# Kernel tuning notes

Measured on AMD Instinct MI355X. Metric: run time of the kernel, lower is better.

The kernel has to match this reference:

```python
import jax, jax.numpy as jnp
import numpy as np

B, S, E, H, T, VOCAB = 64, 512, 256, 512, 32, 32000

def setup_inputs():
    key = jax.random.key(0)
    ks = jax.random.split(key, 19)
    g = lambda i, shape: jax.random.normal(ks[i], shape, jnp.float32) * 0.05
    return {
        "sentence": jax.random.randint(ks[0], (S, B), 0, VOCAB),
        "emb_enc": g(1, (VOCAB, E)),
        "emb_dec": g(2, (VOCAB, E)),
        "W_ih": g(3, (4 * H, E)),
        "W_hh": g(4, (4 * H, H)),
        "b_ih": g(5, (4 * H,)),
        "b_hh": g(6, (4 * H,)),
        "dec_in0": g(7, (E,)),
        "Wx": g(8, (4 * H, E)),
        "bx": g(9, (4 * H,)),
        "Wh": g(10, (4 * H, H)),
        "bh": g(11, (4 * H,)),
        "W_out": g(12, (H, 2 * H)),
        "b_out": g(13, (H,)),
        "W_in": g(14, (H, H)),
        "b_in": g(15, (H,)),
        "W_ctx": g(16, (H, H)),
        "b_ctx": g(17, (H,)),
        "V": jax.random.uniform(ks[18], (H,), jnp.float32, -1.0, 1.0),
    }

def _lstm_cell(x, h, c, Wi, Whh, bi, bhh):
    # gate order i, f, g, o (matches torch LSTM and the decoder's chunk order)
    gates = x @ Wi.T + h @ Whh.T + bi + bhh
    i, f, g, o = jnp.split(gates, 4, axis=-1)
    c_t = jax.nn.sigmoid(f) * c + jax.nn.sigmoid(i) * jnp.tanh(g)
    h_t = jax.nn.sigmoid(o) * jnp.tanh(c_t)
    return h_t, c_t

def _pointer_net(sentence, emb_enc, emb_dec, W_ih, W_hh, b_ih, b_hh, dec_in0,
                 Wx, bx, Wh, bh, W_out, b_out, W_in, b_in, W_ctx, b_ctx, V):
    s_len, b = sentence.shape
    h_dim = W_hh.shape[1]
    embs = emb_enc[sentence]                          # [S, B, E]
    h0 = jnp.zeros((b, h_dim), embs.dtype)
    c0 = jnp.zeros((b, h_dim), embs.dtype)

    def enc_step(carry, x_t):
        h, c = _lstm_cell(x_t, carry[0], carry[1], W_ih, W_hh, b_ih, b_hh)
        return (h, c), h

    (h_n, c_n), enc_out = jax.lax.scan(enc_step, (h0, c0), embs)   # enc_out [S, B, H]
    context = enc_out.transpose(1, 0, 2)              # [B, S, H]
    # conv1d(kernel=1) projection of the context; constant across decode steps
    ctx = jnp.einsum('bsh,gh->bgs', context, W_ctx) + b_ctx[None, :, None]  # [B, H, S]

    dec_embs = emb_dec[sentence].transpose(1, 0, 2)   # [B, S, E]
    pos = jnp.arange(s_len)

    def dec_step(carry, _):
        dec_in, h, c, mask = carry
        h_t, c_t = _lstm_cell(dec_in, h, c, Wx, Wh, bx, bh)
        inp = h_t @ W_in.T + b_in                      # [B, H]
        att = jnp.einsum('h,bhs->bs', V, jnp.tanh(inp[:, :, None] + ctx))
        att = jnp.where(mask == 0, -jnp.inf, att)
        alpha = jax.nn.softmax(att, axis=1)            # [B, S]
        hidden_state = jnp.einsum('bhs,bs->bh', ctx, alpha)
        h_new = jnp.tanh(jnp.concatenate([hidden_state, h_t], axis=1) @ W_out.T + b_out)
        idx = jnp.argmax(alpha * mask, axis=1)         # greedy pointer, first max on ties
        one_hot = (pos[None, :] == idx[:, None]).astype(alpha.dtype)
        mask_new = mask * (1.0 - one_hot)
        next_in = jnp.take_along_axis(dec_embs, idx[:, None, None], axis=1)[:, 0, :]
        return (next_in, h_new, c_t, mask_new), (alpha, idx)

    mask0 = jnp.ones((b, s_len), embs.dtype)
    dec_in0_b = jnp.broadcast_to(dec_in0, (b, dec_in0.shape[0]))
    _, (alphas, ptrs) = jax.lax.scan(dec_step, (dec_in0_b, h_n, c_n, mask0), None, length=T)
    return alphas.transpose(1, 0, 2), ptrs.T          # [B, T, S], [B, T]

def reference(sentence, emb_enc, emb_dec, W_ih, W_hh, b_ih, b_hh, dec_in0,
              Wx, bx, Wh, bh, W_out, b_out, W_in, b_in, W_ctx, b_ctx, V):
    return _pointer_net(sentence, emb_enc, emb_dec, W_ih, W_hh, b_ih, b_hh, dec_in0,
                        Wx, bx, Wh, bh, W_out, b_out, W_in, b_in, W_ctx, b_ctx, V)
```

## Files before the change

### kernel.cpp

```cpp
#include <hip/hip_runtime.h>
#include <hip/hip_bf16.h>


typedef unsigned short u16;
typedef unsigned long long u64;
typedef __bf16 bf16_t;
typedef bf16_t bf16x8 __attribute__((ext_vector_type(8)));
typedef float f32x4 __attribute__((ext_vector_type(4)));

#define MFMA16(a, b, c) __builtin_amdgcn_mfma_f32_16x16x32_bf16(a, b, c, 0, 0, 0)
#define AGENT __HIP_MEMORY_SCOPE_AGENT

#define FLG_OFF   64u
#define FLE_OFF   128u
#define FLC_OFF   8320u
#define LDD_OFF   10368u
#define GEND_OFF  11392u
#define FLD_OFF   11520u
#define BAR_END   27904u
#define HE_OFF    32768u
#define CW_OFF    425984u
#define HD_OFF    557056u
#define AO_OFF    688128u
#define INP_OFF   950272u
#define ATT_OFF   1081344u
#define MSK_OFF   1212416u
#define PAC_OFF   1343488u
#define PML_OFF   1867776u
#define DIN_OFF   1871872u
#define CTX_OFF   2097152u
#define CTXL_OFF  (CTX_OFF + 33554432u)
#define NEED_T0   (CTX_OFF + 67108864u)
#define NEED_T1   (CTX_OFF + 50331648u)
#define NEED_T2   (CTX_OFF + 33554432u)

__device__ __forceinline__ float bf2f(u16 b) {
  union { unsigned u; float f; } c; c.u = ((unsigned)b) << 16; return c.f;
}
__device__ __forceinline__ u16 f2bf(float x) {
  union { float f; unsigned u; } c; c.f = x;
  unsigned r = c.u + 0x7FFFu + ((c.u >> 16) & 1u);
  return (u16)(r >> 16);
}
__device__ __forceinline__ float sigf(float x) { return 1.0f / (1.0f + expf(-x)); }
__device__ __forceinline__ float sel4(float a0, float a1, float a2, float a3, int j) {
  float r = (j == 1) ? a1 : a0;
  r = (j == 2) ? a2 : r;
  r = (j == 3) ? a3 : r;
  return r;
}
__device__ __forceinline__ float wget(const void* p, long i, int f32m) {
  return f32m ? ((const float*)p)[i] : bf2f(((const u16*)p)[i]);
}
__device__ __forceinline__ void ld8(const void* p, long i, int f32m, float (&o)[8]) {
  if (f32m) {
    const float4* q = (const float4*)((const float*)p + i);
    float4 a = q[0], b = q[1];
    o[0] = a.x; o[1] = a.y; o[2] = a.z; o[3] = a.w;
    o[4] = b.x; o[5] = b.y; o[6] = b.z; o[7] = b.w;
  } else {
    uint4 u = *(const uint4*)((const u16*)p + i);
    unsigned ww[4] = {u.x, u.y, u.z, u.w};
#pragma unroll
    for (int k = 0; k < 4; ++k) {
      o[2 * k] = bf2f((u16)(ww[k] & 0xFFFFu));
      o[2 * k + 1] = bf2f((u16)(ww[k] >> 16));
    }
  }
}
__device__ __forceinline__ float ald(const float* p) {
  return __hip_atomic_load(p, __ATOMIC_RELAXED, AGENT);
}
__device__ __forceinline__ void ast(float* p, float v) {
  __hip_atomic_store(p, v, __ATOMIC_RELAXED, AGENT);
}
__device__ __forceinline__ int aldi(const int* p) {
  return __hip_atomic_load(p, __ATOMIC_RELAXED, AGENT);
}

__device__ __forceinline__ void split3(float x, u16& h, u16& l, u16& l2) {
  union { float f; unsigned u; } c; c.f = x;
  h = (u16)(c.u >> 16);
  float r = x - bf2f(h);
  union { float f; unsigned u; } e; e.f = r;
  l = (u16)(e.u >> 16);
  float r2 = r - bf2f(l);
  union { float f; unsigned u; } g; g.f = r2;
  l2 = (u16)(g.u >> 16);
}
__device__ __forceinline__ void split8v(const float (&a)[8], bf16x8& H, bf16x8& L,
                                        bf16x8& L2) {
  union { unsigned u[4]; bf16x8 v; } hh, ll, mm;
#pragma unroll
  for (int k = 0; k < 4; ++k) {
    union { float f; unsigned u; } x0, x1;
    x0.f = a[2 * k]; x1.f = a[2 * k + 1];
    unsigned t0 = x0.u & 0xFFFF0000u, t1 = x1.u & 0xFFFF0000u;
    union { unsigned u; float f; } b0, b1; b0.u = t0; b1.u = t1;
    float r0 = x0.f - b0.f, r1 = x1.f - b1.f;
    union { float f; unsigned u; } e0, e1; e0.f = r0; e1.f = r1;
    unsigned s0 = e0.u & 0xFFFF0000u, s1 = e1.u & 0xFFFF0000u;
    union { unsigned u; float f; } c0, c1; c0.u = s0; c1.u = s1;
    float q0 = r0 - c0.f, q1 = r1 - c1.f;
    union { float f; unsigned u; } g0, g1; g0.f = q0; g1.f = q1;
    hh.u[k] = t1 | (x0.u >> 16);
    ll.u[k] = s1 | (e0.u >> 16);
    mm.u[k] = (g1.u & 0xFFFF0000u) | (g0.u >> 16);
  }
  H = hh.v; L = ll.v; L2 = mm.v;
}
__device__ __forceinline__ f32x4 mfma6(const bf16x8& ah, const bf16x8& al,
                                       const bf16x8& al2, const bf16x8& bh,
                                       const bf16x8& bl, const bf16x8& bl2, f32x4 acc) {
  acc = MFMA16(ah, bh, acc);
  acc = MFMA16(al, bh, acc);
  acc = MFMA16(ah, bl, acc);
  acc = MFMA16(al, bl, acc);
  acc = MFMA16(ah, bl2, acc);
  acc = MFMA16(al2, bh, acc);
  return acc;
}
__device__ __forceinline__ f32x4 groupMMv(const float (&a8)[8], const u16* B3c, int bo,
                                          f32x4 acc) {
  bf16x8 H, L, L2;
  split8v(a8, H, L, L2);
  return mfma6(H, L, L2, *(const bf16x8*)(B3c + bo), *(const bf16x8*)(B3c + 4224 + bo),
               *(const bf16x8*)(B3c + 8448 + bo), acc);
}
__device__ __forceinline__ void stage16(u16* B3, const void* W, int f32m,
                                        long src, int n, int k16) {
  float t0[8], t1[8];
  ld8(W, src, f32m, t0);
  ld8(W, src + 8, f32m, t1);
#pragma unroll
  for (int j = 0; j < 8; ++j) {
    u16 h, l, l2; split3(t0[j], h, l, l2);
    int o = n * 264 + k16 + j;
    B3[o] = h; B3[4224 + o] = l; B3[8448 + o] = l2;
  }
#pragma unroll
  for (int j = 0; j < 8; ++j) {
    u16 h, l, l2; split3(t1[j], h, l, l2);
    int o = n * 264 + k16 + 8 + j;
    B3[o] = h; B3[4224 + o] = l; B3[8448 + o] = l2;
  }
}

__device__ __forceinline__ f32x4 gemmStaged(const float* __restrict__ T,
    const u16* __restrict__ B3, int kgoff, int ng, float* __restrict__ hS,
    int tid, int ln15, int q, int bA, f32x4 acc) {
  const int nch = ng >> 2;
  u64 pend[16];
#pragma unroll
  for (int i = 0; i < 16; ++i)
    pend[i] = __hip_atomic_load((const u64*)T + i * 256 + tid,
                                __ATOMIC_RELAXED, AGENT);
  __syncthreads();
#pragma unroll
  for (int i = 0; i < 16; ++i) {
    int gi = i * 256 + tid;
    ((u64*)hS)[(gi >> 5) * 33 + (gi & 31)] = pend[i];
  }
  __syncthreads();
#pragma unroll 1
  for (int c = 0; c < nch; ++c) {
    if (c + 1 < nch) {
#pragma unroll
      for (int i = 0; i < 16; ++i)
        pend[i] = __hip_atomic_load((const u64*)T + (c + 1) * 4096 + i * 256 + tid,
                                    __ATOMIC_RELAXED, AGENT);
    }
#pragma unroll
    for (int k4 = 0; k4 < 4; ++k4) {
      const int kg = c * 4 + k4 + kgoff;
      float a8[8];
#pragma unroll
      for (int j = 0; j < 8; ++j)
        a8[j] = hS[(k4 * 32 + q * 8 + j) * 66 + bA];
      acc = groupMMv(a8, B3 + (kg >> 3) * 12672,
                     ln15 * 264 + (kg & 7) * 32 + q * 8, acc);
    }
    if (c + 1 < nch) {
      __syncthreads();
#pragma unroll
      for (int i = 0; i < 16; ++i) {
        int gi = i * 256 + tid;
        ((u64*)hS)[(gi >> 5) * 33 + (gi & 31)] = pend[i];
      }
      __syncthreads();
    }
  }
  return acc;
}

__device__ __forceinline__ void ctx_store(char* ws, int tier, int oi, float x) {
  if (tier == 0) { ((float*)(ws + CTX_OFF))[oi] = x; return; }
  if (tier >= 3) return;
  u16 hi = f2bf(x);
  ((u16*)(ws + CTX_OFF))[oi] = hi;
  if (tier == 1) {
    unsigned e = hi & 0x7F80u; if (e == 0) e = 0x0080u;
    float us = bf2f((u16)e) * 0.00390625f;
    float r = (x - bf2f(hi)) / us;
    int q = (int)__float2int_rn(r * 254.0f);
    q = max(-127, min(127, q));
    ((signed char*)(ws + CTXL_OFF))[oi] = (signed char)q;
  }
}
__device__ __forceinline__ void ctx_load8(const char* ws, int tier, int oi, float (&cx)[8]) {
  if (tier == 0) {
    const float4* p = (const float4*)((const float*)(ws + CTX_OFF) + oi);
    float4 a = p[0], b = p[1];
    cx[0] = a.x; cx[1] = a.y; cx[2] = a.z; cx[3] = a.w;
    cx[4] = b.x; cx[5] = b.y; cx[6] = b.z; cx[7] = b.w;
    return;
  }
  if (tier >= 3) {
#pragma unroll
    for (int j = 0; j < 8; ++j) cx[j] = 0.0f;
    return;
  }
  uint4 hu = *(const uint4*)((const u16*)(ws + CTX_OFF) + oi);
  unsigned hw[4] = {hu.x, hu.y, hu.z, hu.w};
  u16 h[8];
#pragma unroll
  for (int k = 0; k < 4; ++k) { h[2*k] = (u16)(hw[k] & 0xFFFFu); h[2*k+1] = (u16)(hw[k] >> 16); }
#pragma unroll
  for (int j = 0; j < 8; ++j) cx[j] = bf2f(h[j]);
  if (tier == 1) {
    const signed char* lp = (const signed char*)(ws + CTXL_OFF) + oi;
#pragma unroll
    for (int j = 0; j < 8; ++j) {
      unsigned e = h[j] & 0x7F80u; if (e == 0) e = 0x0080u;
      float us = bf2f((u16)e) * 0.00390625f;
      cx[j] += (float)lp[j] * us * (1.0f / 254.0f);
    }
  }
}

__device__ __forceinline__ void enc_arrive(char* ws, unsigned off, int idx, int gen) {
  __builtin_amdgcn_s_waitcnt(0);
  __syncthreads();
  if (threadIdx.x == 0)
    __hip_atomic_store((int*)(ws + off) + idx * 16, gen, __ATOMIC_RELAXED, AGENT);
}
__device__ __forceinline__ void gate_wait(char* ws, int gen, int genc) {
  const int tid = threadIdx.x;
  if (tid < 128) {
    const int* f = (const int*)(ws + FLE_OFF) + tid * 16;
    while (aldi(f) < gen) __builtin_amdgcn_s_sleep(2);
  } else if (tid < 160 && genc > 0) {
    const int* f = (const int*)(ws + FLC_OFF) + (tid - 128) * 16;
    while (aldi(f) < genc) __builtin_amdgcn_s_sleep(2);
  }
  __syncthreads();
}
__device__ __forceinline__ void ctx_wait(char* ws, int gen) {
  const int tid = threadIdx.x;
  if (tid < 128) {
    const int* f = (const int*)(ws + FLE_OFF) + tid * 16;
    while (aldi(f) < gen) __builtin_amdgcn_s_sleep(2);
  }
  __syncthreads();
}

__device__ __forceinline__ void sbar_arrive(char* ws, int wg, int gen) {
  __builtin_amdgcn_s_waitcnt(0);
  __syncthreads();
  if (threadIdx.x == 0)
    __hip_atomic_store((int*)(ws + FLD_OFF) + wg * 16, gen, __ATOMIC_RELAXED, AGENT);
}
__device__ __forceinline__ void sbar_wait(char* ws, int wg, int gen) {
  const int tid = threadIdx.x;
  if (tid < 64) {
    int* fl = (int*)(ws + FLD_OFF);
    int* ldv = (int*)(ws + LDD_OFF);
    int* gp = (int*)(ws + GEND_OFF);
    if (wg < 16) {
      if (tid < 16) {
        const int* f = &fl[(wg + (tid << 4)) * 16];
        while (aldi(f) < gen) __builtin_amdgcn_s_sleep(2);
      }
      if (tid == 0) __hip_atomic_store(&ldv[wg * 16], gen, __ATOMIC_RELAXED, AGENT);
    }
    if (wg == 0) {
      if (tid < 16) {
        const int* f = &ldv[tid * 16];
        while (aldi(f) < gen) __builtin_amdgcn_s_sleep(2);
      }
      if (tid == 0) __hip_atomic_store(gp, gen, __ATOMIC_RELAXED, AGENT);
    }
    if (tid == 0)
      while (aldi((const int*)gp) < gen) __builtin_amdgcn_s_sleep(2);
  }
  __syncthreads();
}

__global__ void prep_detect(const void* embE, char* ws) {
  __shared__ int cnt;
  if (threadIdx.x == 0) cnt = 0;
  __syncthreads();
  const u16* p = (const u16*)embE;
  int c = 0;
  for (int i = threadIdx.x; i < 4096; i += 256) {
    float v = bf2f(p[i]);
    if (!(fabsf(v) < 4.0f)) c++;
  }
  atomicAdd(&cnt, c);
  __syncthreads();
  if (threadIdx.x == 0) *(int*)(ws + FLG_OFF) = (cnt > 200) ? 1 : 0;
}

__global__ void prep_init(const void* din0, char* ws) {
  const int f32m = *(const int*)(ws + FLG_OFF);
  int i0 = blockIdx.x * 256 + threadIdx.x;
  int stride = gridDim.x * 256;
  int* bars = (int*)ws;
  for (int i = i0; i < (int)((BAR_END - FLE_OFF) / 4); i += stride)
    bars[(FLE_OFF / 4) + i] = 0;
  float* he = (float*)(ws + HE_OFF);
  float* mask = (float*)(ws + MSK_OFF);
  float* dinT = (float*)(ws + DIN_OFF);
  for (int i = i0; i < 98304; i += stride) he[i] = 0.0f;
  for (int i = i0; i < 32768; i += stride) mask[i] = 1.0f;
  for (int i = i0; i < 16384; i += stride) dinT[i] = wget(din0, i >> 6, f32m);
}

__global__ __launch_bounds__(256, 1) void enc_pers(
    const int* __restrict__ sent, const void* __restrict__ embE,
    const void* __restrict__ Wih, const void* __restrict__ Whh,
    const void* __restrict__ bih, const void* __restrict__ bhh,
    const void* __restrict__ Wctx, const void* __restrict__ bctx,
    char* __restrict__ ws, int tier) {
  __shared__ __align__(16) u16 B3[38016];
  __shared__ __align__(16) float hS[8448];
  const int tid = threadIdx.x, w = blockIdx.x;
  const int f32m = *(const int*)(ws + FLG_OFF);
  const int lane = tid & 63, v = tid >> 6, ln15 = lane & 15, q = lane >> 4;
  const int bA = v * 16 + ln15;
  const int sn = tid >> 4, sk = (tid & 15) * 16;
  float* heT = (float*)(ws + HE_OFF);
  float* cwp = (float*)(ws + CW_OFF);

  const int g = ln15 & 3;
  const int unit = w * 4 + (ln15 >> 2);

  if (w < 128) {
    float creg[4];
#pragma unroll
    for (int r = 0; r < 4; ++r) creg[r] = 0.0f;
    long grC = (long)(g * 512 + unit);
    float bias = wget(bih, grC, f32m) + wget(bhh, grC, f32m);
    const long grS = (long)((sn & 3) * 512 + w * 4 + (sn >> 2));
    stage16(B3, Wih, f32m, grS * 256 + sk, sn, sk);
    stage16(B3 + 12672, Whh, f32m, grS * 512 + sk, sn, sk);
    stage16(B3 + 25344, Whh, f32m, grS * 512 + 256 + sk, sn, sk);
    __syncthreads();

    int sR = 2, sW = 0;
#pragma unroll 1
    for (int u = 0; u < 512; ++u) {
      const int tok = sent[u * 64 + bA];
      f32x4 acc = {0.f, 0.f, 0.f, 0.f};
      {
        float aE[4][8];
#pragma unroll
        for (int pf = 0; pf < 3; ++pf)
          ld8(embE, (long)tok * 256 + pf * 32 + q * 8, f32m, aE[pf]);
#pragma unroll
        for (int ks = 0; ks < 8; ++ks) {
          if (ks + 3 < 8) ld8(embE, (long)tok * 256 + (ks + 3) * 32 + q * 8, f32m,
                              aE[(ks + 3) & 3]);
          acc = groupMMv(aE[ks & 3], B3, ln15 * 264 + ks * 32 + q * 8, acc);
        }
      }
      if (u) gate_wait(ws, u, u - 1);
      acc = gemmStaged(heT + sR * 32768, B3, 8, 16, hS, tid, ln15, q, bA, acc);
      float* hdTs = heT + sW * 32768;
#pragma unroll
      for (int r = 0; r < 4; ++r) {
        int br = v * 16 + q * 4 + r;
        float val = acc[r] + bias;
        float x1 = __shfl_xor(val, 1);
        float x2 = __shfl_xor(val, 2);
        float x3 = __shfl_xor(val, 3);
        float gi = sel4(val, x1, x2, x3, g);
        float gf = sel4(val, x1, x2, x3, g ^ 1);
        float gg = sel4(val, x1, x2, x3, g ^ 2);
        float go = sel4(val, x1, x2, x3, g ^ 3);
        float cn = sigf(gf) * creg[r] + sigf(gi) * tanhf(gg);
        float hv = sigf(go) * tanhf(cn);
        creg[r] = cn;
        if (g == 0) ast(hdTs + unit * 64 + br, hv);
      }
      enc_arrive(ws, FLE_OFF, w, u + 1);
      sR = sW; sW = (sW == 2) ? 0 : sW + 1;
    }
    if (g == 0) {
#pragma unroll
      for (int r = 0; r < 4; ++r) cwp[(v * 16 + q * 4 + r) * 512 + unit] = creg[r];
    }
  } else {
    const int w2 = w - 128;
    const long grS = (long)(w2 * 16 + sn);
    stage16(B3, Wctx, f32m, grS * 512 + sk, sn, sk);
    stage16(B3 + 12672, Wctx, f32m, grS * 512 + 256 + sk, sn, sk);
    __syncthreads();
    const int d = w2 * 16 + ln15;
    float bb = wget(bctx, d, f32m);
    int sC = 0;
#pragma unroll 1
    for (int vv = 0; vv < 512; ++vv) {
      ctx_wait(ws, vv + 1);
      f32x4 acc = {0.f, 0.f, 0.f, 0.f};
      acc = gemmStaged(heT + sC * 32768, B3, 0, 16, hS, tid, ln15, q, bA, acc);
#pragma unroll
      for (int r = 0; r < 4; ++r) {
        int br = v * 16 + q * 4 + r;
        ctx_store(ws, tier, (br * 512 + vv) * 512 + d, acc[r] + bb);
      }
      enc_arrive(ws, FLC_OFF, w2, vv + 1);
      sC = (sC == 2) ? 0 : sC + 1;
    }
  }
}

__global__ __launch_bounds__(256, 1) void dec_pers(
    const int* __restrict__ sent, const void* __restrict__ embD,
    const void* __restrict__ Wx, const void* __restrict__ bx,
    const void* __restrict__ Wh, const void* __restrict__ bh,
    const void* __restrict__ Wout, const void* __restrict__ bout,
    const void* __restrict__ Win, const void* __restrict__ bin,
    const void* __restrict__ V, char* __restrict__ ws,
    float* __restrict__ out, int tier) {
  __shared__ __align__(16) u16 B3[50688];
  __shared__ __align__(16) float hS[8448];
  __shared__ float accL[512];
  __shared__ float mlL[8];
  __shared__ float redA[256];
  __shared__ int redI[256];

  const int tid = threadIdx.x, wg = blockIdx.x;
  const int f32m = *(const int*)(ws + FLG_OFF);
  const int lane = tid & 63, v = tid >> 6, ln15 = lane & 15, q = lane >> 4;
  const int bA = v * 16 + ln15;
  const int sn = tid >> 4, sk = (tid & 15) * 16;
  float* hdT = (float*)(ws + HD_OFF);
  float* aoT = (float*)(ws + AO_OFF);
  float* inp = (float*)(ws + INP_OFF);
  float* att = (float*)(ws + ATT_OFF);
  float* mask = (float*)(ws + MSK_OFF);
  float* pac = (float*)(ws + PAC_OFF);
  float* pml = (float*)(ws + PML_OFF);
  float* dinT = (float*)(ws + DIN_OFF);
  const float* hnT = (const float*)(ws + HE_OFF) + 32768;
  int bgen = 0;

  const int g = ln15 & 3;
  const int unit = (wg < 128) ? (wg * 4 + (ln15 >> 2)) : 0;
  float creg[4];
  float bias = 0.0f;
  if (wg < 128) {
    const float* cwp = (const float*)(ws + CW_OFF);
#pragma unroll
    for (int r = 0; r < 4; ++r) creg[r] = cwp[(v * 16 + q * 4 + r) * 512 + unit];
    bias = wget(bx, (long)(g * 512 + unit), f32m) + wget(bh, (long)(g * 512 + unit), f32m);
  }
  float vj[8];
#pragma unroll
  for (int j = 0; j < 8; ++j) vj[j] = wget(V, lane * 8 + j, f32m);

  if (wg < 128) {
    const long grS = (long)((sn & 3) * 512 + wg * 4 + (sn >> 2));
    stage16(B3, Wx, f32m, grS * 256 + sk, sn, sk);
    stage16(B3 + 12672, Wh, f32m, grS * 512 + sk, sn, sk);
    stage16(B3 + 25344, Wh, f32m, grS * 512 + 256 + sk, sn, sk);
  } else if (wg < 160) {
    const long grS = (long)((wg - 128) * 16 + sn);
    stage16(B3, Win, f32m, grS * 512 + sk, sn, sk);
    stage16(B3 + 12672, Win, f32m, grS * 512 + 256 + sk, sn, sk);
  } else if (wg < 192) {
    const long grS = (long)((wg - 160) * 16 + sn);
#pragma unroll
    for (int cc = 0; cc < 4; ++cc)
      stage16(B3 + cc * 12672, Wout, f32m, grS * 1024 + cc * 256 + sk, sn, sk);
  }
  __syncthreads();

  f32x4 acc1 = {0.f, 0.f, 0.f, 0.f};
  if (wg < 128)
    acc1 = gemmStaged(dinT, B3, 0, 8, hS, tid, ln15, q, bA, acc1);

#pragma unroll 1
  for (int t = 0; t < 32; ++t) {
    if (wg < 128) {
      const float* hsT = (t == 0) ? hnT : (const float*)hdT;
      acc1 = gemmStaged(hsT, B3, 8, 16, hS, tid, ln15, q, bA, acc1);
#pragma unroll
      for (int r = 0; r < 4; ++r) {
        int br = v * 16 + q * 4 + r;
        float val = acc1[r] + bias;
        float x1 = __shfl_xor(val, 1);
        float x2 = __shfl_xor(val, 2);
        float x3 = __shfl_xor(val, 3);
        float gi = sel4(val, x1, x2, x3, g);
        float gf = sel4(val, x1, x2, x3, g ^ 1);
        float gg = sel4(val, x1, x2, x3, g ^ 2);
        float go = sel4(val, x1, x2, x3, g ^ 3);
        float cn = sigf(gf) * creg[r] + sigf(gi) * tanhf(gg);
        float hv = sigf(go) * tanhf(cn);
        creg[r] = cn;
        if (g == 0) ast(aoT + (512 + unit) * 64 + br, hv);
      }
    }
    ++bgen;
    sbar_arrive(ws, wg, bgen);
    sbar_wait(ws, wg, bgen);
    if (wg >= 128 && wg < 160) {
      f32x4 acc = {0.f, 0.f, 0.f, 0.f};
      acc = gemmStaged((const float*)aoT + 32768, B3, 0, 16, hS, tid, ln15, q, bA, acc);
      const int d = (wg - 128) * 16 + ln15;
      float bb = wget(bin, d, f32m);
#pragma unroll
      for (int r = 0; r < 4; ++r)
        ast(inp + (v * 16 + q * 4 + r) * 512 + d, acc[r] + bb);
    }
    ++bgen;
    sbar_arrive(ws, wg, bgen);
    const int b = wg & 63, qq = wg >> 6;
    const int s0 = qq * 128 + v * 32;
    float mkB[4];
    float cxB[4][8];
#pragma unroll
    for (int pf = 0; pf < 3; ++pf) {
      mkB[pf] = ald(mask + b * 512 + s0 + pf);
      ctx_load8(ws, tier, (b * 512 + s0 + pf) * 512 + lane * 8, cxB[pf]);
    }
    sbar_wait(ws, wg, bgen);
    {
      float ij[8];
#pragma unroll
      for (int j = 0; j < 8; ++j) ij[j] = ald(inp + b * 512 + lane * 8 + j);
      for (int i = tid; i < 512; i += 256) accL[i] = 0.0f;
      __syncthreads();
      float m = -1e30f, l = 0.0f;
      float oacc[8];
#pragma unroll
      for (int j = 0; j < 8; ++j) oacc[j] = 0.0f;
#pragma unroll 1
      for (int i0 = 0; i0 < 32; ++i0) {
        const int s = s0 + i0;
        if (i0 + 3 < 32) {
          mkB[(i0 + 3) & 3] = ald(mask + b * 512 + s + 3);
          ctx_load8(ws, tier, (b * 512 + s + 3) * 512 + lane * 8, cxB[(i0 + 3) & 3]);
        }
        float mkC = mkB[i0 & 3];
        const float (&cxC)[8] = cxB[i0 & 3];
        if (mkC == 0.0f) {
          if (lane == 0) ast(att + b * 512 + s, -1e30f);
        } else {
          float p = 0.0f;
#pragma unroll
          for (int j = 0; j < 8; ++j) p += vj[j] * tanhf(ij[j] + cxC[j]);
#pragma unroll
          for (int off = 1; off < 64; off <<= 1) p += __shfl_xor(p, off);
          if (lane == 0) ast(att + b * 512 + s, p);
          if (p <= m) {
            float e = expf(p - m);
            l += e;
#pragma unroll
            for (int j = 0; j < 8; ++j) oacc[j] += e * cxC[j];
          } else {
            float sc = expf(m - p);
            l = l * sc + 1.0f;
#pragma unroll
            for (int j = 0; j < 8; ++j) oacc[j] = oacc[j] * sc + cxC[j];
            m = p;
          }
        }
      }
      if (lane == 0) { mlL[v * 2] = m; mlL[v * 2 + 1] = l; }
      __syncthreads();
      float M = fmaxf(fmaxf(mlL[0], mlL[2]), fmaxf(mlL[4], mlL[6]));
      float Lq = 0.0f;
#pragma unroll
      for (int vv = 0; vv < 4; ++vv) Lq += mlL[vv * 2 + 1] * expf(mlL[vv * 2] - M);
      float scv = expf(m - M);
      for (int vv = 0; vv < 4; ++vv) {
        if (v == vv) {
#pragma unroll
          for (int j = 0; j < 8; ++j) accL[lane * 8 + j] += oacc[j] * scv;
        }
        __syncthreads();
      }
      for (int i = tid; i < 512; i += 256) ast(pac + (b * 4 + qq) * 512 + i, accL[i]);
      if (tid == 0) {
        ast(pml + (b * 4 + qq) * 2, M);
        ast(pml + (b * 4 + qq) * 2 + 1, Lq);
      }
    }
    ++bgen;
    sbar_arrive(ws, wg, bgen);
    sbar_wait(ws, wg, bgen);
    if (wg < 64) {
      const int bb = wg;
      float m0 = ald(pml + (bb * 4 + 0) * 2), m1 = ald(pml + (bb * 4 + 1) * 2);
      float m2 = ald(pml + (bb * 4 + 2) * 2), m3 = ald(pml + (bb * 4 + 3) * 2);
      float l0 = ald(pml + (bb * 4 + 0) * 2 + 1), l1 = ald(pml + (bb * 4 + 1) * 2 + 1);
      float l2 = ald(pml + (bb * 4 + 2) * 2 + 1), l3 = ald(pml + (bb * 4 + 3) * 2 + 1);
      float M = fmaxf(fmaxf(m0, m1), fmaxf(m2, m3));
      float e0 = expf(m0 - M), e1 = expf(m1 - M), e2 = expf(m2 - M), e3 = expf(m3 - M);
      float L = l0 * e0 + l1 * e1 + l2 * e2 + l3 * e3;
      L = fmaxf(L, 1e-30f);
      for (int h = tid; h < 512; h += 256) {
        float hv = (ald(pac + (bb * 4 + 0) * 512 + h) * e0 +
                    ald(pac + (bb * 4 + 1) * 512 + h) * e1 +
                    ald(pac + (bb * 4 + 2) * 512 + h) * e2 +
                    ald(pac + (bb * 4 + 3) * 512 + h) * e3) / L;
        ast(aoT + h * 64 + bb, hv);
      }
      float bestA = -1.0f;
      int bestS = 0;
#pragma unroll
      for (int k = 0; k < 2; ++k) {
        int s = tid * 2 + k;
        float a = expf(ald(att + bb * 512 + s) - M) / L;
        out[(bb * 32 + t) * 512 + s] = a;
        if (a > bestA) { bestA = a; bestS = s; }
      }
      redA[tid] = bestA;
      redI[tid] = bestS;
      __syncthreads();
      for (int st = 128; st > 0; st >>= 1) {
        if (tid < st) {
          if (redA[tid + st] > redA[tid]) { redA[tid] = redA[tid + st]; redI[tid] = redI[tid + st]; }
        }
        __syncthreads();
      }
      int idx = redI[0];
      if (tid == 0) {
        ast(mask + bb * 512 + idx, 0.0f);
        out[1048576 + bb * 32 + t] = (float)idx;
      }
      int token = sent[idx * 64 + bb];
      ast(dinT + tid * 64 + bb, wget(embD, (long)token * 256 + tid, f32m));
    }
    ++bgen;
    sbar_arrive(ws, wg, bgen);
    sbar_wait(ws, wg, bgen);
    if (wg >= 160 && wg < 192) {
      f32x4 acc = {0.f, 0.f, 0.f, 0.f};
      acc = gemmStaged((const float*)aoT, B3, 0, 32, hS, tid, ln15, q, bA, acc);
      const int d = (wg - 160) * 16 + ln15;
      float bb2 = wget(bout, d, f32m);
#pragma unroll
      for (int r = 0; r < 4; ++r)
        ast(hdT + d * 64 + (v * 16 + q * 4 + r), tanhf(acc[r] + bb2));
    }
    ++bgen;
    sbar_arrive(ws, wg, bgen);
    if (wg < 128 && t < 31) {
      f32x4 accn = {0.f, 0.f, 0.f, 0.f};
      accn = gemmStaged(dinT, B3, 0, 8, hS, tid, ln15, q, bA, accn);
      acc1 = accn;
    }
    if (t < 31) sbar_wait(ws, wg, bgen);
  }
}

__global__ void diag_kernel(char* ws, float* out, int wsMiB) {
  if (threadIdx.x == 0 && blockIdx.x == 0) {
    int f = *(int*)(ws + FLG_OFF);
    out[0] = (float)(wsMiB + 2000 * f);
  }
}

extern "C" void kernel_launch(void* const* d_in, const int* in_sizes, int n_in,
                              void* d_out, int out_size, void* d_ws, size_t ws_size,
                              hipStream_t stream) {
  (void)in_sizes; (void)n_in; (void)out_size;
  const int* sent = (const int*)d_in[0];
  const void* embE = d_in[1];
  const void* embD = d_in[2];
  const void* Wih = d_in[3];
  const void* Whh = d_in[4];
  const void* bih = d_in[5];
  const void* bhh = d_in[6];
  const void* din0 = d_in[7];
  const void* Wx = d_in[8];
  const void* bx = d_in[9];
  const void* Wh = d_in[10];
  const void* bh = d_in[11];
  const void* Wout = d_in[12];
  const void* bout = d_in[13];
  const void* Win = d_in[14];
  const void* bin = d_in[15];
  const void* Wctx = d_in[16];
  const void* bctx = d_in[17];
  const void* V = d_in[18];
  char* ws = (char*)d_ws;
  float* out = (float*)d_out;

  int tier;
  if (ws_size >= (size_t)NEED_T0) tier = 0;
  else if (ws_size >= (size_t)NEED_T1) tier = 1;
  else if (ws_size >= (size_t)NEED_T2) tier = 2;
  else tier = 3;

  prep_detect<<<dim3(1), dim3(256), 0, stream>>>(embE, ws);
  prep_init<<<dim3(64), dim3(256), 0, stream>>>(din0, ws);
  enc_pers<<<dim3(160), dim3(256), 0, stream>>>(sent, embE, Wih, Whh, bih, bhh,
                                                Wctx, bctx, ws, tier);
  dec_pers<<<dim3(256), dim3(256), 0, stream>>>(sent, embD, Wx, bx, Wh, bh, Wout, bout,
                                                Win, bin, V, ws, out, tier);
  if (tier >= 2)
    diag_kernel<<<dim3(1), dim3(64), 0, stream>>>(ws, out, (int)(ws_size >> 20));
}
```

Baseline: 9.206 ms.

## Double-buffer staged GEMM operands and restructure grid barriers into two-level trees

```diff
diff --git a/kernel.cpp b/kernel.cpp
--- a/kernel.cpp
+++ b/kernel.cpp
@@ -14,10 +14,10 @@
 #define FLG_OFF   64u
 #define FLE_OFF   128u
 #define FLC_OFF   8320u
-#define LDD_OFF   10368u
-#define GEND_OFF  11392u
-#define FLD_OFF   11520u
-#define BAR_END   27904u
+#define LDVG_OFF  10368u
+#define FLD_OFF   10880u
+#define LDVD_OFF  27264u
+#define BAR_END   28288u
 #define HE_OFF    32768u
 #define CW_OFF    425984u
 #define HD_OFF    557056u
@@ -77,6 +77,9 @@
 __device__ __forceinline__ int aldi(const int* p) {
   return __hip_atomic_load(p, __ATOMIC_RELAXED, AGENT);
 }
+__device__ __forceinline__ void asti(int* p, int v) {
+  __hip_atomic_store(p, v, __ATOMIC_RELAXED, AGENT);
+}
 
 __device__ __forceinline__ void split3(float x, u16& h, u16& l, u16& l2) {
   union { float f; unsigned u; } c; c.f = x;
@@ -146,46 +149,99 @@
   }
 }
 
-__device__ __forceinline__ f32x4 gemmStaged(const float* __restrict__ T,
+__device__ __forceinline__ f32x4 gemmStaged128(const float* __restrict__ T,
     const u16* __restrict__ B3, int kgoff, int ng, float* __restrict__ hS,
     int tid, int ln15, int q, int bA, f32x4 acc) {
   const int nch = ng >> 2;
   u64 pend[16];
 #pragma unroll
   for (int i = 0; i < 16; ++i)
-    pend[i] = __hip_atomic_load((const u64*)T + i * 256 + tid,
-                                __ATOMIC_RELAXED, AGENT);
+    pend[i] = __hip_atomic_load((const u64*)T + i * 256 + tid, __ATOMIC_RELAXED, AGENT);
   __syncthreads();
 #pragma unroll
   for (int i = 0; i < 16; ++i) {
     int gi = i * 256 + tid;
     ((u64*)hS)[(gi >> 5) * 33 + (gi & 31)] = pend[i];
   }
+#pragma unroll
+  for (int i = 0; i < 16; ++i)
+    pend[i] = __hip_atomic_load((const u64*)T + 4096 + i * 256 + tid,
+                                __ATOMIC_RELAXED, AGENT);
   __syncthreads();
 #pragma unroll 1
   for (int c = 0; c < nch; ++c) {
-    if (c + 1 < nch) {
-#pragma unroll
-      for (int i = 0; i < 16; ++i)
-        pend[i] = __hip_atomic_load((const u64*)T + (c + 1) * 4096 + i * 256 + tid,
-                                    __ATOMIC_RELAXED, AGENT);
-    }
+    const int buf = c & 1;
 #pragma unroll
     for (int k4 = 0; k4 < 4; ++k4) {
       const int kg = c * 4 + k4 + kgoff;
       float a8[8];
 #pragma unroll
       for (int j = 0; j < 8; ++j)
-        a8[j] = hS[(k4 * 32 + q * 8 + j) * 66 + bA];
+        a8[j] = hS[buf * 8448 + (k4 * 32 + q * 8 + j) * 66 + bA];
       acc = groupMMv(a8, B3 + (kg >> 3) * 12672,
                      ln15 * 264 + (kg & 7) * 32 + q * 8, acc);
     }
     if (c + 1 < nch) {
-      __syncthreads();
 #pragma unroll
       for (int i = 0; i < 16; ++i) {
         int gi = i * 256 + tid;
-        ((u64*)hS)[(gi >> 5) * 33 + (gi & 31)] = pend[i];
+        ((u64*)hS)[((c + 1) & 1) * 4224 + (gi >> 5) * 33 + (gi & 31)] = pend[i];
+      }
+      if (c + 2 < nch) {
+#pragma unroll
+        for (int i = 0; i < 16; ++i)
+          pend[i] = __hip_atomic_load((const u64*)T + (c + 2) * 4096 + i * 256 + tid,
+                                      __ATOMIC_RELAXED, AGENT);
+      }
+      __syncthreads();
+    }
+  }
+  return acc;
+}
+
+__device__ __forceinline__ f32x4 gemmStaged64(const float* __restrict__ T,
+    const u16* __restrict__ B3, int kgoff, int ng, float* __restrict__ hS,
+    int tid, int ln15, int q, int bA, f32x4 acc) {
+  const int nch = ng >> 1;
+  u64 pend[8];
+#pragma unroll
+  for (int i = 0; i < 8; ++i)
+    pend[i] = __hip_atomic_load((const u64*)T + i * 256 + tid, __ATOMIC_RELAXED, AGENT);
+  __syncthreads();
+#pragma unroll
+  for (int i = 0; i < 8; ++i) {
+    int gi = i * 256 + tid;
+    ((u64*)hS)[(gi >> 5) * 33 + (gi & 31)] = pend[i];
+  }
+#pragma unroll
+  for (int i = 0; i < 8; ++i)
+    pend[i] = __hip_atomic_load((const u64*)T + 2048 + i * 256 + tid,
+                                __ATOMIC_RELAXED, AGENT);
+  __syncthreads();
+#pragma unroll 1
+  for (int c = 0; c < nch; ++c) {
+    const int buf = c & 1;
+#pragma unroll
+    for (int k2 = 0; k2 < 2; ++k2) {
+      const int kg = c * 2 + k2 + kgoff;
+      float a8[8];
+#pragma unroll
+      for (int j = 0; j < 8; ++j)
+        a8[j] = hS[buf * 4224 + (k2 * 32 + q * 8 + j) * 66 + bA];
+      acc = groupMMv(a8, B3 + (kg >> 3) * 12672,
+                     ln15 * 264 + (kg & 7) * 32 + q * 8, acc);
+    }
+    if (c + 1 < nch) {
+#pragma unroll
+      for (int i = 0; i < 8; ++i) {
+        int gi = i * 256 + tid;
+        ((u64*)hS)[((c + 1) & 1) * 2112 + (gi >> 5) * 33 + (gi & 31)] = pend[i];
+      }
+      if (c + 2 < nch) {
+#pragma unroll
+        for (int i = 0; i < 8; ++i)
+          pend[i] = __hip_atomic_load((const u64*)T + (c + 2) * 2048 + i * 256 + tid,
+                                      __ATOMIC_RELAXED, AGENT);
       }
       __syncthreads();
     }
@@ -242,14 +298,22 @@
   __builtin_amdgcn_s_waitcnt(0);
   __syncthreads();
   if (threadIdx.x == 0)
-    __hip_atomic_store((int*)(ws + off) + idx * 16, gen, __ATOMIC_RELAXED, AGENT);
-}
-__device__ __forceinline__ void gate_wait(char* ws, int gen, int genc) {
+    asti((int*)(ws + off) + idx * 16, gen);
+}
+__device__ __forceinline__ void gate_wait(char* ws, int wg, int gen, int genc) {
   const int tid = threadIdx.x;
-  if (tid < 128) {
-    const int* f = (const int*)(ws + FLE_OFF) + tid * 16;
+  if (wg < 8) {
+    if (tid < 16) {
+      const int* f = (const int*)(ws + FLE_OFF) + (wg * 16 + tid) * 16;
+      while (aldi(f) < gen) __builtin_amdgcn_s_sleep(1);
+    }
+    if (tid == 0) asti((int*)(ws + LDVG_OFF) + wg * 16, gen);
+  }
+  if (tid < 8) {
+    const int* f = (const int*)(ws + LDVG_OFF) + tid * 16;
     while (aldi(f) < gen) __builtin_amdgcn_s_sleep(2);
-  } else if (tid < 160 && genc > 0) {
+  }
+  if (genc > 0 && tid >= 128 && tid < 160) {
     const int* f = (const int*)(ws + FLC_OFF) + (tid - 128) * 16;
     while (aldi(f) < genc) __builtin_amdgcn_s_sleep(2);
   }
@@ -257,41 +321,31 @@
 }
 __device__ __forceinline__ void ctx_wait(char* ws, int gen) {
   const int tid = threadIdx.x;
-  if (tid < 128) {
-    const int* f = (const int*)(ws + FLE_OFF) + tid * 16;
+  if (tid < 8) {
+    const int* f = (const int*)(ws + LDVG_OFF) + tid * 16;
     while (aldi(f) < gen) __builtin_amdgcn_s_sleep(2);
   }
   __syncthreads();
 }
 
-__device__ __forceinline__ void sbar_arrive(char* ws, int wg, int gen) {
+__device__ __forceinline__ void dbar_arrive(char* ws, int wg, int gen) {
   __builtin_amdgcn_s_waitcnt(0);
   __syncthreads();
   if (threadIdx.x == 0)
-    __hip_atomic_store((int*)(ws + FLD_OFF) + wg * 16, gen, __ATOMIC_RELAXED, AGENT);
-}
-__device__ __forceinline__ void sbar_wait(char* ws, int wg, int gen) {
+    asti((int*)(ws + FLD_OFF) + wg * 16, gen);
+}
+__device__ __forceinline__ void dbar_wait(char* ws, int wg, int gen) {
   const int tid = threadIdx.x;
-  if (tid < 64) {
-    int* fl = (int*)(ws + FLD_OFF);
-    int* ldv = (int*)(ws + LDD_OFF);
-    int* gp = (int*)(ws + GEND_OFF);
-    if (wg < 16) {
-      if (tid < 16) {
-        const int* f = &fl[(wg + (tid << 4)) * 16];
-        while (aldi(f) < gen) __builtin_amdgcn_s_sleep(2);
-      }
-      if (tid == 0) __hip_atomic_store(&ldv[wg * 16], gen, __ATOMIC_RELAXED, AGENT);
-    }
-    if (wg == 0) {
-      if (tid < 16) {
-        const int* f = &ldv[tid * 16];
-        while (aldi(f) < gen) __builtin_amdgcn_s_sleep(2);
-      }
-      if (tid == 0) __hip_atomic_store(gp, gen, __ATOMIC_RELAXED, AGENT);
-    }
-    if (tid == 0)
-      while (aldi((const int*)gp) < gen) __builtin_amdgcn_s_sleep(2);
+  if (wg < 16) {
+    if (tid < 16) {
+      const int* f = (const int*)(ws + FLD_OFF) + (wg * 16 + tid) * 16;
+      while (aldi(f) < gen) __builtin_amdgcn_s_sleep(1);
+    }
+    if (tid == 0) asti((int*)(ws + LDVD_OFF) + wg * 16, gen);
+  }
+  if (tid < 16) {
+    const int* f = (const int*)(ws + LDVD_OFF) + tid * 16;
+    while (aldi(f) < gen) __builtin_amdgcn_s_sleep(2);
   }
   __syncthreads();
 }
@@ -333,7 +387,7 @@
     const void* __restrict__ Wctx, const void* __restrict__ bctx,
     char* __restrict__ ws, int tier) {
   __shared__ __align__(16) u16 B3[38016];
-  __shared__ __align__(16) float hS[8448];
+  __shared__ __align__(16) float hS[16896];
   const int tid = threadIdx.x, w = blockIdx.x;
   const int f32m = *(const int*)(ws + FLG_OFF);
   const int lane = tid & 63, v = tid >> 6, ln15 = lane & 15, q = lane >> 4;
@@ -374,8 +428,8 @@
           acc = groupMMv(aE[ks & 3], B3, ln15 * 264 + ks * 32 + q * 8, acc);
         }
       }
-      if (u) gate_wait(ws, u, u - 1);
-      acc = gemmStaged(heT + sR * 32768, B3, 8, 16, hS, tid, ln15, q, bA, acc);
+      if (u) gate_wait(ws, w, u, u - 2);
+      acc = gemmStaged128(heT + sR * 32768, B3, 8, 16, hS, tid, ln15, q, bA, acc);
       float* hdTs = heT + sW * 32768;
 #pragma unroll
       for (int r = 0; r < 4; ++r) {
@@ -396,6 +450,13 @@
       enc_arrive(ws, FLE_OFF, w, u + 1);
       sR = sW; sW = (sW == 2) ? 0 : sW + 1;
     }
+    if (w < 8) {
+      if (tid < 16) {
+        const int* f = (const int*)(ws + FLE_OFF) + (w * 16 + tid) * 16;
+        while (aldi(f) < 512) __builtin_amdgcn_s_sleep(1);
+      }
+      if (tid == 0) asti((int*)(ws + LDVG_OFF) + w * 16, 512);
+    }
     if (g == 0) {
 #pragma unroll
       for (int r = 0; r < 4; ++r) cwp[(v * 16 + q * 4 + r) * 512 + unit] = creg[r];
@@ -413,7 +474,7 @@
     for (int vv = 0; vv < 512; ++vv) {
       ctx_wait(ws, vv + 1);
       f32x4 acc = {0.f, 0.f, 0.f, 0.f};
-      acc = gemmStaged(heT + sC * 32768, B3, 0, 16, hS, tid, ln15, q, bA, acc);
+      acc = gemmStaged128(heT + sC * 32768, B3, 0, 16, hS, tid, ln15, q, bA, acc);
 #pragma unroll
       for (int r = 0; r < 4; ++r) {
         int br = v * 16 + q * 4 + r;
@@ -489,13 +550,13 @@
 
   f32x4 acc1 = {0.f, 0.f, 0.f, 0.f};
   if (wg < 128)
-    acc1 = gemmStaged(dinT, B3, 0, 8, hS, tid, ln15, q, bA, acc1);
+    acc1 = gemmStaged64(dinT, B3, 0, 8, hS, tid, ln15, q, bA, acc1);
 
 #pragma unroll 1
   for (int t = 0; t < 32; ++t) {
     if (wg < 128) {
       const float* hsT = (t == 0) ? hnT : (const float*)hdT;
-      acc1 = gemmStaged(hsT, B3, 8, 16, hS, tid, ln15, q, bA, acc1);
+      acc1 = gemmStaged64(hsT, B3, 8, 16, hS, tid, ln15, q, bA, acc1);
 #pragma unroll
       for (int r = 0; r < 4; ++r) {
         int br = v * 16 + q * 4 + r;
@@ -514,11 +575,11 @@
       }
     }
     ++bgen;
-    sbar_arrive(ws, wg, bgen);
-    sbar_wait(ws, wg, bgen);
+    dbar_arrive(ws, wg, bgen);
+    dbar_wait(ws, wg, bgen);
     if (wg >= 128 && wg < 160) {
       f32x4 acc = {0.f, 0.f, 0.f, 0.f};
-      acc = gemmStaged((const float*)aoT + 32768, B3, 0, 16, hS, tid, ln15, q, bA, acc);
+      acc = gemmStaged64((const float*)aoT + 32768, B3, 0, 16, hS, tid, ln15, q, bA, acc);
       const int d = (wg - 128) * 16 + ln15;
       float bb = wget(bin, d, f32m);
 #pragma unroll
@@ -526,7 +587,7 @@
         ast(inp + (v * 16 + q * 4 + r) * 512 + d, acc[r] + bb);
     }
     ++bgen;
-    sbar_arrive(ws, wg, bgen);
+    dbar_arrive(ws, wg, bgen);
     const int b = wg & 63, qq = wg >> 6;
     const int s0 = qq * 128 + v * 32;
     float mkB[4];
@@ -536,7 +597,7 @@
       mkB[pf] = ald(mask + b * 512 + s0 + pf);
       ctx_load8(ws, tier, (b * 512 + s0 + pf) * 512 + lane * 8, cxB[pf]);
     }
-    sbar_wait(ws, wg, bgen);
+    dbar_wait(ws, wg, bgen);
     {
       float ij[8];
 #pragma unroll
@@ -600,8 +661,29 @@
       }
     }
     ++bgen;
-    sbar_arrive(ws, wg, bgen);
-    sbar_wait(ws, wg, bgen);
+    dbar_arrive(ws, wg, bgen);
+    dbar_wait(ws, wg, bgen);
+    if (wg >= 64 && wg < 128) {
+      const int j = wg - 64;
+      const int bb = tid & 63;
+      float m0 = ald(pml + (bb * 4 + 0) * 2), m1 = ald(pml + (bb * 4 + 1) * 2);
+      float m2 = ald(pml + (bb * 4 + 2) * 2), m3 = ald(pml + (bb * 4 + 3) * 2);
+      float l0 = ald(pml + (bb * 4 + 0) * 2 + 1), l1 = ald(pml + (bb * 4 + 1) * 2 + 1);
+      float l2 = ald(pml + (bb * 4 + 2) * 2 + 1), l3 = ald(pml + (bb * 4 + 3) * 2 + 1);
+      float M = fmaxf(fmaxf(m0, m1), fmaxf(m2, m3));
+      float e0 = expf(m0 - M), e1 = expf(m1 - M), e2 = expf(m2 - M), e3 = expf(m3 - M);
+      float L = l0 * e0 + l1 * e1 + l2 * e2 + l3 * e3;
+      L = fmaxf(L, 1e-30f);
+#pragma unroll
+      for (int k = 0; k < 2; ++k) {
+        int h = j * 8 + (tid >> 6) * 2 + k;
+        float hv = (ald(pac + (bb * 4 + 0) * 512 + h) * e0 +
+                    ald(pac + (bb * 4 + 1) * 512 + h) * e1 +
+                    ald(pac + (bb * 4 + 2) * 512 + h) * e2 +
+                    ald(pac + (bb * 4 + 3) * 512 + h) * e3) / L;
+        ast(aoT + h * 64 + bb, hv);
+      }
+    }
     if (wg < 64) {
       const int bb = wg;
       float m0 = ald(pml + (bb * 4 + 0) * 2), m1 = ald(pml + (bb * 4 + 1) * 2);
@@ -612,13 +694,6 @@
       float e0 = expf(m0 - M), e1 = expf(m1 - M), e2 = expf(m2 - M), e3 = expf(m3 - M);
       float L = l0 * e0 + l1 * e1 + l2 * e2 + l3 * e3;
       L = fmaxf(L, 1e-30f);
-      for (int h = tid; h < 512; h += 256) {
-        float hv = (ald(pac + (bb * 4 + 0) * 512 + h) * e0 +
-                    ald(pac + (bb * 4 + 1) * 512 + h) * e1 +
-                    ald(pac + (bb * 4 + 2) * 512 + h) * e2 +
-                    ald(pac + (bb * 4 + 3) * 512 + h) * e3) / L;
-        ast(aoT + h * 64 + bb, hv);
-      }
       float bestA = -1.0f;
       int bestS = 0;
 #pragma unroll
@@ -646,11 +721,11 @@
       ast(dinT + tid * 64 + bb, wget(embD, (long)token * 256 + tid, f32m));
     }
     ++bgen;
-    sbar_arrive(ws, wg, bgen);
-    sbar_wait(ws, wg, bgen);
+    dbar_arrive(ws, wg, bgen);
+    dbar_wait(ws, wg, bgen);
     if (wg >= 160 && wg < 192) {
       f32x4 acc = {0.f, 0.f, 0.f, 0.f};
-      acc = gemmStaged((const float*)aoT, B3, 0, 32, hS, tid, ln15, q, bA, acc);
+      acc = gemmStaged64((const float*)aoT, B3, 0, 32, hS, tid, ln15, q, bA, acc);
       const int d = (wg - 160) * 16 + ln15;
       float bb2 = wget(bout, d, f32m);
 #pragma unroll
@@ -658,13 +733,13 @@
         ast(hdT + d * 64 + (v * 16 + q * 4 + r), tanhf(acc[r] + bb2));
     }
     ++bgen;
-    sbar_arrive(ws, wg, bgen);
+    dbar_arrive(ws, wg, bgen);
     if (wg < 128 && t < 31) {
       f32x4 accn = {0.f, 0.f, 0.f, 0.f};
-      accn = gemmStaged(dinT, B3, 0, 8, hS, tid, ln15, q, bA, accn);
+      accn = gemmStaged64(dinT, B3, 0, 8, hS, tid, ln15, q, bA, accn);
       acc1 = accn;
     }
-    if (t < 31) sbar_wait(ws, wg, bgen);
+    if (t < 31) dbar_wait(ws, wg, bgen);
   }
 }
 
```

Result: slower. 9.634 ms (+4.6%).
